# Kernel optimization log

Hardware: AMD Instinct MI355X
Metric: run time of the kernel (lower is better)

Reference implementation:

```python
import jax, jax.numpy as jnp
import numpy as np

D = 64          # lrp_out_dim
L = 16          # lrp_length
LEN_SEQ = 4     # int(sqrt(L))
N = 200000      # nodes
E = 800000      # edges
NPERM = 250000  # permutation patterns
P = NPERM * L   # perm slots (sparse matrix rows)
G = 4096        # graphs (pooling output rows)


def _spmm(row, col, val, m, dense):
    # sparse [m, n] @ dense [n, d] via gather + segment_sum
    return jax.ops.segment_sum(val[:, None] * dense[col], row, num_segments=m)


def setup_inputs() -> dict:
    key = jax.random.key(0)
    ks = jax.random.split(key, 16)
    x = jax.random.normal(ks[0], (N, D), jnp.float32)
    efeat = jax.random.normal(ks[1], (E, D), jnp.float32)
    degs = jax.random.uniform(ks[2], (N,), jnp.float32) * 8.0
    n2p_row = jax.random.randint(ks[3], (P,), 0, P)
    n2p_col = jax.random.randint(ks[4], (P,), 0, N)
    n2p_val = jax.random.uniform(ks[5], (P,), jnp.float32)
    e2p_row = jax.random.randint(ks[6], (P,), 0, P)
    e2p_col = jax.random.randint(ks[7], (P,), 0, E)
    e2p_val = jax.random.uniform(ks[8], (P,), jnp.float32)
    pool_row = jax.random.randint(ks[9], (NPERM,), 0, G)
    pool_col = jax.random.randint(ks[10], (NPERM,), 0, NPERM)
    pool_val = jnp.ones((NPERM,), jnp.float32)
    weights = jax.random.normal(ks[11], (D, D, L), jnp.float32)
    bias = jnp.zeros((1, D), jnp.float32)
    W0 = jax.random.normal(ks[12], (2 * D, LEN_SEQ), jnp.float32) * 0.1
    b0 = jnp.zeros((2 * D,), jnp.float32)
    W1 = jax.random.normal(ks[13], (D, 2 * D), jnp.float32) * 0.1
    b1 = jnp.zeros((D,), jnp.float32)
    Wl = jax.random.normal(ks[14], (D, D), jnp.float32) * 0.1
    bl = jnp.zeros((D,), jnp.float32)
    return dict(x=x, efeat=efeat, degs=degs,
                n2p_row=n2p_row, n2p_col=n2p_col, n2p_val=n2p_val,
                e2p_row=e2p_row, e2p_col=e2p_col, e2p_val=e2p_val,
                pool_row=pool_row, pool_col=pool_col, pool_val=pool_val,
                weights=weights, bias=bias, W0=W0, b0=b0, W1=W1, b1=b1,
                Wl=Wl, bl=bl)


def reference(x, efeat, degs,
              n2p_row, n2p_col, n2p_val,
              e2p_row, e2p_col, e2p_val,
              pool_row, pool_col, pool_val,
              weights, bias, W0, b0, W1, b1, Wl, bl):
    # permutation gather of node and edge features into perm slots: [P, D]
    nfeat = _spmm(n2p_row, n2p_col, n2p_val, P, x) \
          + _spmm(e2p_row, e2p_col, e2p_val, P, efeat)
    deg_perm = _spmm(n2p_row, n2p_col, n2p_val, P, degs[:, None])  # [P, 1]
    # transpose->view->permute in torch is equivalent to a plain reshape here
    nfeat = nfeat.reshape(NPERM, L, D)           # [n_perms, L, D]
    # diagonal-position degree entries: columns 0, 5, 10, 15
    deg_perm = deg_perm.reshape(NPERM, L)[:, jnp.arange(0, L, LEN_SEQ + 1)]  # [n_perms, 4]
    # einsum 'dab,bca->dc' with nfeat [n, a=L, b=D], weights [b=D, c=D, a=L]
    h = jnp.einsum('nlb,bcl->nc', nfeat, weights) + bias
    h = jax.nn.relu(h) @ Wl.T + bl               # self.linear(relu(...))
    dg = jax.nn.relu(deg_perm @ W0.T + b0) @ W1.T + b1  # degree MLP gate
    out = h * dg                                  # [n_perms, D]
    return _spmm(pool_row, pool_col, pool_val, G, out)  # [G, D]
```

## Files before the change

### kernel.cpp

```cpp
#include <hip/hip_runtime.h>

#define NPERM_C 250000
#define P_C     4000000
#define G_C     4096
#define NB1     1954
#define NB2     123

typedef __attribute__((ext_vector_type(8))) short bf16x8;
typedef __attribute__((ext_vector_type(4))) float f32x4;

static __device__ __forceinline__ unsigned short f2bf(float f) {
    unsigned u = __float_as_uint(f);
    unsigned r = (u + 0x7fffu + ((u >> 16) & 1u)) >> 16;
    return (unsigned short)r;
}
static __device__ __forceinline__ float bf2f(unsigned short s) {
    return __uint_as_float(((unsigned)s) << 16);
}

__global__ void repack_bpk(const float* __restrict__ w, unsigned short* __restrict__ bpk) {
    int o = blockIdx.x * 256 + threadIdx.x;
    int j = o & 7, lane = (o >> 3) & 63, h = (o >> 9) & 1;
    int nt = (o >> 10) & 3, ks = (o >> 12) & 1, l = o >> 13;
    int b = ks * 32 + (lane >> 4) * 8 + j;
    int c = nt * 16 + (lane & 15);
    float wv = w[(b * 64 + c) * 16 + l];
    unsigned short hb = f2bf(wv);
    bpk[o] = (h == 0) ? hb : f2bf(wv - bf2f(hb));
}

__global__ void repack_wlpk(const float* __restrict__ wl, unsigned short* __restrict__ wpk) {
    int o = blockIdx.x * 256 + threadIdx.x;
    int j = o & 7, lane = (o >> 3) & 63, h = (o >> 9) & 1;
    int nt = (o >> 10) & 3, ks = o >> 12;
    int k = ks * 32 + (lane >> 4) * 8 + j;
    int c2 = nt * 16 + (lane & 15);
    float wv = wl[c2 * 64 + k];
    unsigned short hb = f2bf(wv);
    wpk[o] = (h == 0) ? hb : f2bf(wv - bf2f(hb));
}

__global__ __launch_bounds__(256) void pool_hist(const int* __restrict__ pcol,
                                                 int* __restrict__ poolCnt) {
    int i = blockIdx.x * 256 + threadIdx.x;
    if (i < NPERM_C) atomicAdd(&poolCnt[pcol[i]], 1);
}

__global__ __launch_bounds__(256) void pool_scan_local(const int* __restrict__ poolCnt,
                                                       int* __restrict__ poolRank,
                                                       int* __restrict__ bsum2) {
    __shared__ int ts[256];
    int b = blockIdx.x, t = threadIdx.x;
    int base = b * 2048 + t * 8;
    int v[8]; int s = 0;
#pragma unroll
    for (int i = 0; i < 8; ++i) {
        int idx = base + i;
        v[i] = (idx < NPERM_C) ? (poolCnt[idx] != 0) : 0;
        s += v[i];
    }
    ts[t] = s;
    __syncthreads();
    for (int ofs = 1; ofs < 256; ofs <<= 1) {
        int xv = (t >= ofs) ? ts[t - ofs] : 0;
        __syncthreads();
        ts[t] += xv;
        __syncthreads();
    }
    int run = ts[t] - s;
    if (t == 255) bsum2[b] = ts[255];
#pragma unroll
    for (int i = 0; i < 8; ++i) {
        int idx = base + i;
        if (idx < NPERM_C) poolRank[idx] = run;
        run += v[i];
    }
}

__global__ void pool_scan_top(int* __restrict__ bsum2) {
    __shared__ int ts[256];
    int t = threadIdx.x;
    int v = (t < NB2) ? bsum2[t] : 0;
    ts[t] = v;
    __syncthreads();
    for (int ofs = 1; ofs < 256; ofs <<= 1) {
        int xv = (t >= ofs) ? ts[t - ofs] : 0;
        __syncthreads();
        ts[t] += xv;
        __syncthreads();
    }
    if (t < NB2) bsum2[t] = ts[t] - v;
}

__global__ __launch_bounds__(256) void pool_scan_add(const int* __restrict__ poolCnt,
                                                     int* __restrict__ poolRank,
                                                     const int* __restrict__ bsum2,
                                                     int* __restrict__ act,
                                                     int* __restrict__ nActB) {
    int b = blockIdx.x, t = threadIdx.x;
    int add = bsum2[b];
    int base = b * 2048 + t * 8;
#pragma unroll
    for (int i = 0; i < 8; ++i) {
        int idx = base + i;
        if (idx < NPERM_C) {
            int flag = poolCnt[idx] != 0;
            int o = poolRank[idx] + add;
            poolRank[idx] = o;
            if (flag) act[o] = idx;
            if (idx == NPERM_C - 1) nActB[0] = o + flag;
        }
    }
}

__global__ __launch_bounds__(256) void hist(const int* __restrict__ r1,
                                            const int* __restrict__ r2,
                                            const int* __restrict__ poolCnt,
                                            int* __restrict__ cnt) {
    int i = blockIdx.x * 256 + threadIdx.x;
    int r;
    if (i < P_C)            r = r1[i];
    else if (i < 2 * P_C)   r = r2[i - P_C];
    else return;
    if (poolCnt[r >> 4] != 0) atomicAdd(&cnt[r], 1);
}

__global__ __launch_bounds__(256) void scan_local(const int* __restrict__ cnt,
                                                  int* __restrict__ off,
                                                  int* __restrict__ bsum) {
    __shared__ int ts[256];
    int b = blockIdx.x, t = threadIdx.x;
    int base = b * 2048 + t * 8;
    int v[8]; int s = 0;
#pragma unroll
    for (int i = 0; i < 8; ++i) {
        int idx = base + i;
        v[i] = (idx < P_C) ? cnt[idx] : 0;
        s += v[i];
    }
    ts[t] = s;
    __syncthreads();
    for (int ofs = 1; ofs < 256; ofs <<= 1) {
        int xv = (t >= ofs) ? ts[t - ofs] : 0;
        __syncthreads();
        ts[t] += xv;
        __syncthreads();
    }
    int run = ts[t] - s;
    if (t == 255) bsum[b] = ts[255];
#pragma unroll
    for (int i = 0; i < 8; ++i) {
        int idx = base + i;
        if (idx < P_C) off[idx] = run;
        run += v[i];
    }
}

__global__ void scan_top(int* __restrict__ bsum) {
    __shared__ int ts[256];
    int t = threadIdx.x;
    int base = t * 8;
    int v[8]; int s = 0;
#pragma unroll
    for (int i = 0; i < 8; ++i) {
        int idx = base + i;
        v[i] = (idx < NB1) ? bsum[idx] : 0;
        s += v[i];
    }
    ts[t] = s;
    __syncthreads();
    for (int ofs = 1; ofs < 256; ofs <<= 1) {
        int xv = (t >= ofs) ? ts[t - ofs] : 0;
        __syncthreads();
        ts[t] += xv;
        __syncthreads();
    }
    int run = ts[t] - s;
#pragma unroll
    for (int i = 0; i < 8; ++i) {
        int idx = base + i;
        if (idx < NB1) bsum[idx] = run;
        run += v[i];
    }
}

__global__ __launch_bounds__(256) void scan_add(int* __restrict__ off,
                                                const int* __restrict__ bsum,
                                                int* __restrict__ cur) {
    int b = blockIdx.x, t = threadIdx.x;
    int add = bsum[b];
    int base = b * 2048 + t * 8;
#pragma unroll
    for (int i = 0; i < 8; ++i) {
        int idx = base + i;
        if (idx < P_C) {
            int o = off[idx] + add;
            if (idx == P_C - 1) off[P_C] = o + cur[idx];
            off[idx] = o;
            cur[idx] = o;
        }
    }
}

__global__ __launch_bounds__(256) void scat(
        const int* __restrict__ r1, const int* __restrict__ c1, const float* __restrict__ v1,
        const int* __restrict__ r2, const int* __restrict__ c2, const float* __restrict__ v2,
        const int* __restrict__ poolCnt,
        int* __restrict__ cur, uint2* __restrict__ suv) {
    int i = blockIdx.x * 256 + threadIdx.x;
    int row; unsigned key; float val;
    if (i < P_C)          { row = r1[i]; key = (unsigned)c1[i]; val = v1[i]; }
    else if (i < 2 * P_C) { int j = i - P_C; row = r2[j]; key = (unsigned)c2[j] | 0x100000u; val = v2[j]; }
    else return;
    if (poolCnt[row >> 4] == 0) return;
    int pos = atomicAdd(&cur[row], 1);
    suv[pos] = make_uint2(key, __float_as_uint(val));
}

__global__ __launch_bounds__(256) void gather_nfeat(
        const uint2* __restrict__ suv, const int* __restrict__ pOff,
        const float* __restrict__ x, const float* __restrict__ efeat,
        const float* __restrict__ degs, const int* __restrict__ act,
        const int* __restrict__ nActB,
        unsigned short* __restrict__ nfH, unsigned short* __restrict__ nfL,
        float* __restrict__ degD, int row0, int rows) {
    int nAct = nActB[0];
    int t = threadIdx.x;
    int w = t >> 6, lane = t & 63;
    int g = lane >> 4, t16 = lane & 15;
    int cr = row0 + blockIdx.x * 2 + (w >> 1);
    int rend = row0 + rows; if (rend > nAct) rend = nAct;
    if (cr >= rend) return;
    int arow = act[cr];
    int posA = (w & 1) * 8 + g * 2;
    int posB = posA + 1;
    int sA = arow * 16 + posA;
    int iA = pOff[sA];
    int eA = pOff[sA + 1];
    int iB = eA;
    int eB = pOff[sA + 2];
    bool needA = (posA == 0) || (posA == 10);
    bool needB = (posB == 5) || (posB == 15);
    float4 aA = {0.f, 0.f, 0.f, 0.f}, aB = {0.f, 0.f, 0.f, 0.f};
    float dA = 0.f, dB = 0.f;
    while ((iA < eA) || (iB < eB)) {
        bool hA = iA < eA, hB = iB < eB;
        uint2 kvA, kvB;
        if (hA) kvA = suv[iA];
        if (hB) kvB = suv[iB];
        if (hA) {
            unsigned k = kvA.x; float v = __uint_as_float(kvA.y);
            const float* f = (k & 0x100000u) ? efeat : x;
            float4 fv = *reinterpret_cast<const float4*>(
                f + (size_t)(k & 0xFFFFFu) * 64 + t16 * 4);
            aA.x = fmaf(v, fv.x, aA.x); aA.y = fmaf(v, fv.y, aA.y);
            aA.z = fmaf(v, fv.z, aA.z); aA.w = fmaf(v, fv.w, aA.w);
            if (needA && !(k & 0x100000u)) dA = fmaf(v, degs[k & 0xFFFFFu], dA);
            ++iA;
        }
        if (hB) {
            unsigned k = kvB.x; float v = __uint_as_float(kvB.y);
            const float* f = (k & 0x100000u) ? efeat : x;
            float4 fv = *reinterpret_cast<const float4*>(
                f + (size_t)(k & 0xFFFFFu) * 64 + t16 * 4);
            aB.x = fmaf(v, fv.x, aB.x); aB.y = fmaf(v, fv.y, aB.y);
            aB.z = fmaf(v, fv.z, aB.z); aB.w = fmaf(v, fv.w, aB.w);
            if (needB && !(k & 0x100000u)) dB = fmaf(v, degs[k & 0xFFFFFu], dB);
            ++iB;
        }
    }
    size_t o = ((size_t)(cr - row0) * 16 + posA) * 64 + t16 * 4;
    ushort4 h4, l4;
    h4.x = f2bf(aA.x); l4.x = f2bf(aA.x - bf2f(h4.x));
    h4.y = f2bf(aA.y); l4.y = f2bf(aA.y - bf2f(h4.y));
    h4.z = f2bf(aA.z); l4.z = f2bf(aA.z - bf2f(h4.z));
    h4.w = f2bf(aA.w); l4.w = f2bf(aA.w - bf2f(h4.w));
    *reinterpret_cast<ushort4*>(nfH + o) = h4;
    *reinterpret_cast<ushort4*>(nfL + o) = l4;
    h4.x = f2bf(aB.x); l4.x = f2bf(aB.x - bf2f(h4.x));
    h4.y = f2bf(aB.y); l4.y = f2bf(aB.y - bf2f(h4.y));
    h4.z = f2bf(aB.z); l4.z = f2bf(aB.z - bf2f(h4.z));
    h4.w = f2bf(aB.w); l4.w = f2bf(aB.w - bf2f(h4.w));
    *reinterpret_cast<ushort4*>(nfH + o + 64) = h4;
    *reinterpret_cast<ushort4*>(nfL + o + 64) = l4;
    if (t16 == 0) {
        if (needA) degD[(size_t)cr * 4 + posA / 5] = dA;
        if (needB) degD[(size_t)cr * 4 + posB / 5] = dB;
    }
}

__global__ __launch_bounds__(256) void dg_gemm(
        const float* __restrict__ degD,
        const float* __restrict__ W0, const float* __restrict__ b0,
        const float* __restrict__ W1, const float* __restrict__ b1,
        const int* __restrict__ nActB,
        float* __restrict__ dgb, int r0, int rows) {
    __shared__ float hidT[128][68];
    __shared__ float w1T[128][68];
    __shared__ float dloc[64][4];
    __shared__ float w0s[128][5];
    int nAct = nActB[0];
    int rend = r0 + rows; if (rend > nAct) rend = nAct;
    int t = threadIdx.x;
    int m0 = r0 + blockIdx.x * 64;
    if (m0 >= rend) return;

    {
        int r = t >> 2, j = t & 3;
        int gr = m0 + r; if (gr >= rend) gr = rend - 1;
        dloc[r][j] = degD[(size_t)gr * 4 + j];
    }
    if (t < 128) {
        w0s[t][0] = W0[t * 4 + 0]; w0s[t][1] = W0[t * 4 + 1];
        w0s[t][2] = W0[t * 4 + 2]; w0s[t][3] = W0[t * 4 + 3];
        w0s[t][4] = b0[t];
    }
    for (int s = 0; s < 32; ++s) {
        int idx = t + s * 256;
        w1T[idx & 127][idx >> 7] = W1[idx];
    }
    __syncthreads();
    for (int s = 0; s < 32; ++s) {
        int idx = t + s * 256;
        int h = idx & 127, r = idx >> 7;
        float v = w0s[h][4] + dloc[r][0] * w0s[h][0] + dloc[r][1] * w0s[h][1]
                            + dloc[r][2] * w0s[h][2] + dloc[r][3] * w0s[h][3];
        hidT[h][r] = fmaxf(v, 0.f);
    }
    __syncthreads();

    int tm = t >> 4, tn = t & 15;
    float acc[4][4] = {};
#pragma unroll 8
    for (int k = 0; k < 128; ++k) {
        float4 a = *reinterpret_cast<const float4*>(&hidT[k][tm * 4]);
        float4 b = *reinterpret_cast<const float4*>(&w1T[k][tn * 4]);
        acc[0][0] = fmaf(a.x, b.x, acc[0][0]); acc[0][1] = fmaf(a.x, b.y, acc[0][1]);
        acc[0][2] = fmaf(a.x, b.z, acc[0][2]); acc[0][3] = fmaf(a.x, b.w, acc[0][3]);
        acc[1][0] = fmaf(a.y, b.x, acc[1][0]); acc[1][1] = fmaf(a.y, b.y, acc[1][1]);
        acc[1][2] = fmaf(a.y, b.z, acc[1][2]); acc[1][3] = fmaf(a.y, b.w, acc[1][3]);
        acc[2][0] = fmaf(a.z, b.x, acc[2][0]); acc[2][1] = fmaf(a.z, b.y, acc[2][1]);
        acc[2][2] = fmaf(a.z, b.z, acc[2][2]); acc[2][3] = fmaf(a.z, b.w, acc[2][3]);
        acc[3][0] = fmaf(a.w, b.x, acc[3][0]); acc[3][1] = fmaf(a.w, b.y, acc[3][1]);
        acc[3][2] = fmaf(a.w, b.z, acc[3][2]); acc[3][3] = fmaf(a.w, b.w, acc[3][3]);
    }
    float bb[4] = {b1[tn * 4 + 0], b1[tn * 4 + 1], b1[tn * 4 + 2], b1[tn * 4 + 3]};
#pragma unroll
    for (int i = 0; i < 4; ++i) {
        int grow = m0 + tm * 4 + i;
        if (grow < rend) {
            float4 o = {acc[i][0] + bb[0], acc[i][1] + bb[1],
                        acc[i][2] + bb[2], acc[i][3] + bb[3]};
            *reinterpret_cast<float4*>(&dgb[(size_t)grow * 64 + tn * 4]) = o;
        }
    }
}

__global__ __launch_bounds__(256) void gemm_mfma(
        const unsigned short* __restrict__ nfH, const unsigned short* __restrict__ nfL,
        const unsigned short* __restrict__ Bpk, const unsigned short* __restrict__ Wlpk,
        const float* __restrict__ bias, const float* __restrict__ bl,
        const float* __restrict__ dgb, const int* __restrict__ nActB,
        float* __restrict__ outb, int r0, int rows) {
    __shared__ unsigned short Hh[128][72];
    __shared__ unsigned short Hl[128][72];
    int nAct = nActB[0];
    int rowsEff = rows; if (r0 + rowsEff > nAct) rowsEff = nAct - r0;
    int t = threadIdx.x, lane = t & 63, w = t >> 6;
    int m0 = blockIdx.x * 128;
    if (m0 >= rowsEff) return;
    int r16 = lane & 15, kg = lane >> 4;

    f32x4 acc[2][4];
#pragma unroll
    for (int i = 0; i < 2; ++i)
#pragma unroll
        for (int j = 0; j < 4; ++j) acc[i][j] = (f32x4){0.f, 0.f, 0.f, 0.f};

    for (int l = 0; l < 16; ++l) {
#pragma unroll
        for (int ks = 0; ks < 2; ++ks) {
            bf16x8 ah[2], al[2];
#pragma unroll
            for (int mt = 0; mt < 2; ++mt) {
                int lr = m0 + w * 32 + mt * 16 + r16;
                if (lr >= rowsEff) lr = rowsEff - 1;
                size_t off = ((size_t)lr * 16 + l) * 64 + ks * 32 + kg * 8;
                ah[mt] = *reinterpret_cast<const bf16x8*>(nfH + off);
                al[mt] = *reinterpret_cast<const bf16x8*>(nfL + off);
            }
#pragma unroll
            for (int nt = 0; nt < 4; ++nt) {
                const unsigned short* bb =
                    Bpk + (size_t)(((l * 2 + ks) * 4 + nt) * 2) * 512 + lane * 8;
                bf16x8 bh = *reinterpret_cast<const bf16x8*>(bb);
                bf16x8 blo = *reinterpret_cast<const bf16x8*>(bb + 512);
#pragma unroll
                for (int mt = 0; mt < 2; ++mt) {
                    acc[mt][nt] = __builtin_amdgcn_mfma_f32_16x16x32_bf16(ah[mt], bh,  acc[mt][nt], 0, 0, 0);
                    acc[mt][nt] = __builtin_amdgcn_mfma_f32_16x16x32_bf16(ah[mt], blo, acc[mt][nt], 0, 0, 0);
                    acc[mt][nt] = __builtin_amdgcn_mfma_f32_16x16x32_bf16(al[mt], bh,  acc[mt][nt], 0, 0, 0);
                }
            }
        }
    }

#pragma unroll
    for (int mt = 0; mt < 2; ++mt)
#pragma unroll
        for (int nt = 0; nt < 4; ++nt) {
            int col = nt * 16 + r16;
            float bv = bias[col];
#pragma unroll
            for (int reg = 0; reg < 4; ++reg) {
                int rl = w * 32 + mt * 16 + kg * 4 + reg;
                float h = fmaxf(acc[mt][nt][reg] + bv, 0.f);
                unsigned short hb = f2bf(h);
                Hh[rl][col] = hb;
                Hl[rl][col] = f2bf(h - bf2f(hb));
            }
        }
    __syncthreads();

    f32x4 acc2[2][4];
#pragma unroll
    for (int i = 0; i < 2; ++i)
#pragma unroll
        for (int j = 0; j < 4; ++j) acc2[i][j] = (f32x4){0.f, 0.f, 0.f, 0.f};

#pragma unroll
    for (int ks = 0; ks < 2; ++ks) {
        bf16x8 ah[2], al[2];
#pragma unroll
        for (int mt = 0; mt < 2; ++mt) {
            int rl = w * 32 + mt * 16 + r16;
            ah[mt] = *reinterpret_cast<const bf16x8*>(&Hh[rl][ks * 32 + kg * 8]);
            al[mt] = *reinterpret_cast<const bf16x8*>(&Hl[rl][ks * 32 + kg * 8]);
        }
#pragma unroll
        for (int nt = 0; nt < 4; ++nt) {
            const unsigned short* wb =
                Wlpk + (size_t)(((ks * 4 + nt) * 2)) * 512 + lane * 8;
            bf16x8 bh = *reinterpret_cast<const bf16x8*>(wb);
            bf16x8 blo = *reinterpret_cast<const bf16x8*>(wb + 512);
#pragma unroll
            for (int mt = 0; mt < 2; ++mt) {
                acc2[mt][nt] = __builtin_amdgcn_mfma_f32_16x16x32_bf16(ah[mt], bh,  acc2[mt][nt], 0, 0, 0);
                acc2[mt][nt] = __builtin_amdgcn_mfma_f32_16x16x32_bf16(ah[mt], blo, acc2[mt][nt], 0, 0, 0);
                acc2[mt][nt] = __builtin_amdgcn_mfma_f32_16x16x32_bf16(al[mt], bh,  acc2[mt][nt], 0, 0, 0);
            }
        }
    }

#pragma unroll
    for (int mt = 0; mt < 2; ++mt)
#pragma unroll
        for (int nt = 0; nt < 4; ++nt) {
            int col = nt * 16 + r16;
            float bv = bl[col];
#pragma unroll
            for (int reg = 0; reg < 4; ++reg) {
                int rl = w * 32 + mt * 16 + kg * 4 + reg;
                if (m0 + rl < rowsEff) {
                    size_t idx = (size_t)(r0 + m0 + rl) * 64 + col;
                    outb[idx] = (acc2[mt][nt][reg] + bv) * dgb[idx];
                }
            }
        }
}

__global__ __launch_bounds__(256) void pool_scatter(
        const int* __restrict__ prow, const int* __restrict__ pcol,
        const float* __restrict__ pval, const int* __restrict__ poolRank,
        const float* __restrict__ outb, float* __restrict__ out) {
    int t = blockIdx.x * 256 + threadIdx.x;
    int i = t >> 6, d = t & 63;
    if (i >= NPERM_C) return;
    int r = prow[i], c = pcol[i];
    float v = pval[i];
    int cr = poolRank[c];
    atomicAdd(&out[(size_t)r * 64 + d], v * outb[(size_t)cr * 64 + d]);
}

extern "C" void kernel_launch(void* const* d_in, const int* in_sizes, int n_in,
                              void* d_out, int out_size, void* d_ws, size_t ws_size,
                              hipStream_t stream) {
    const float* x       = (const float*)d_in[0];
    const float* efeat   = (const float*)d_in[1];
    const float* degs    = (const float*)d_in[2];
    const int*   n2p_row = (const int*)d_in[3];
    const int*   n2p_col = (const int*)d_in[4];
    const float* n2p_val = (const float*)d_in[5];
    const int*   e2p_row = (const int*)d_in[6];
    const int*   e2p_col = (const int*)d_in[7];
    const float* e2p_val = (const float*)d_in[8];
    const int*   pool_row = (const int*)d_in[9];
    const int*   pool_col = (const int*)d_in[10];
    const float* pool_val = (const float*)d_in[11];
    const float* weights = (const float*)d_in[12];
    const float* bias    = (const float*)d_in[13];
    const float* W0      = (const float*)d_in[14];
    const float* b0      = (const float*)d_in[15];
    const float* W1      = (const float*)d_in[16];
    const float* b1      = (const float*)d_in[17];
    const float* Wl      = (const float*)d_in[18];
    const float* bl      = (const float*)d_in[19];
    float* out = (float*)d_out;

    uint2* suv      = (uint2*)d_ws;
    int*   pOff     = (int*)(suv + 8000000);
    int*   pCur     = pOff + 4000064;
    int*   bsum     = pCur + 4000000;
    int*   poolCnt  = bsum + 2048;
    int*   poolRank = poolCnt + 250000;
    int*   act      = poolRank + 250000;
    int*   bsum2    = act + 250000;
    int*   nActB    = bsum2 + 256;
    unsigned short* Bpk  = (unsigned short*)(nActB + 16);
    unsigned short* Wlpk = Bpk + 131072;
    float* degD = (float*)(Wlpk + 8192);
    float* dgb  = degD + 1000000;
    float* outb = dgb;
    unsigned short* nfH = (unsigned short*)(dgb + 16000000);

    const long long base_elems = 16000000LL + 4000064 + 4000000 + 2048 +
                                 250000 * 3 + 256 + 16 + 65536 + 4096 +
                                 1000000 + 16000000;
    long long availf = (long long)(ws_size / 4) - base_elems;
    long long chl = availf / 1024;
    if (chl > NPERM_C) chl = NPERM_C;
    int CH = (int)(chl & ~127LL);
    if (CH < 128) {
        hipMemsetAsync(d_out, 0, (size_t)out_size * 4, stream);
        return;
    }
    unsigned short* nfL = nfH + (size_t)CH * 1024;

    hipMemsetAsync(pCur, 0, (size_t)P_C * 4, stream);
    hipMemsetAsync(poolCnt, 0, (size_t)NPERM_C * 4, stream);
    hipMemsetAsync(out, 0, (size_t)G_C * 64 * 4, stream);

    repack_bpk<<<512, 256, 0, stream>>>(weights, Bpk);
    repack_wlpk<<<32, 256, 0, stream>>>(Wl, Wlpk);

    pool_hist<<<(NPERM_C + 255) / 256, 256, 0, stream>>>(pool_col, poolCnt);
    pool_scan_local<<<NB2, 256, 0, stream>>>(poolCnt, poolRank, bsum2);
    pool_scan_top<<<1, 256, 0, stream>>>(bsum2);
    pool_scan_add<<<NB2, 256, 0, stream>>>(poolCnt, poolRank, bsum2, act, nActB);

    hist<<<31250, 256, 0, stream>>>(n2p_row, e2p_row, poolCnt, pCur);
    scan_local<<<NB1, 256, 0, stream>>>(pCur, pOff, bsum);
    scan_top<<<1, 256, 0, stream>>>(bsum);
    scan_add<<<NB1, 256, 0, stream>>>(pOff, bsum, pCur);
    scat<<<31250, 256, 0, stream>>>(n2p_row, n2p_col, n2p_val,
                                    e2p_row, e2p_col, e2p_val,
                                    poolCnt, pCur, suv);

    for (int c0 = 0; c0 < NPERM_C; c0 += CH) {
        int rows = NPERM_C - c0; if (rows > CH) rows = CH;
        gather_nfeat<<<(rows + 1) / 2, 256, 0, stream>>>(
            suv, pOff, x, efeat, degs, act, nActB, nfH, nfL, degD, c0, rows);
        dg_gemm<<<(rows + 63) / 64, 256, 0, stream>>>(
            degD, W0, b0, W1, b1, nActB, dgb, c0, rows);
        gemm_mfma<<<(rows + 127) / 128, 256, 0, stream>>>(
            nfH, nfL, Bpk, Wlpk, bias, bl, dgb, nActB, outb, c0, rows);
    }

    pool_scatter<<<62500, 256, 0, stream>>>(pool_row, pool_col, pool_val,
                                            poolRank, outb, out);
}
```

Measured before the change: 1.494 ms.

## Balance gather_nfeat work per perm row using shared-memory atomic accumulation

gather_nfeat now processes 8 perm rows per block. Each row's full nonzero range is split across two 16-lane groups, which accumulate into a 32KB shared-memory tile with LDS float atomics instead of per-slot register accumulators. The goal is to remove the load imbalance of the old one-group-per-two-slots loop, where lanes idled while the longest slot finished. The cost is shared atomics, a linear scan to find each entry's slot, more LDS per block (so lower occupancy), and extra block-wide syncs.

```diff
diff --git a/kernel.cpp b/kernel.cpp
--- a/kernel.cpp
+++ b/kernel.cpp
@@ -224,68 +224,75 @@
         const int* __restrict__ nActB,
         unsigned short* __restrict__ nfH, unsigned short* __restrict__ nfL,
         float* __restrict__ degD, int row0, int rows) {
+    __shared__ float accS[8192];
+    __shared__ int   offS[8][17];
+    __shared__ int   arowS[8];
+    __shared__ float degS[8][4];
     int nAct = nActB[0];
     int t = threadIdx.x;
-    int w = t >> 6, lane = t & 63;
-    int g = lane >> 4, t16 = lane & 15;
-    int cr = row0 + blockIdx.x * 2 + (w >> 1);
+    int cr0 = row0 + blockIdx.x * 8;
     int rend = row0 + rows; if (rend > nAct) rend = nAct;
-    if (cr >= rend) return;
-    int arow = act[cr];
-    int posA = (w & 1) * 8 + g * 2;
-    int posB = posA + 1;
-    int sA = arow * 16 + posA;
-    int iA = pOff[sA];
-    int eA = pOff[sA + 1];
-    int iB = eA;
-    int eB = pOff[sA + 2];
-    bool needA = (posA == 0) || (posA == 10);
-    bool needB = (posB == 5) || (posB == 15);
-    float4 aA = {0.f, 0.f, 0.f, 0.f}, aB = {0.f, 0.f, 0.f, 0.f};
-    float dA = 0.f, dB = 0.f;
-    while ((iA < eA) || (iB < eB)) {
-        bool hA = iA < eA, hB = iB < eB;
-        uint2 kvA, kvB;
-        if (hA) kvA = suv[iA];
-        if (hB) kvB = suv[iB];
-        if (hA) {
-            unsigned k = kvA.x; float v = __uint_as_float(kvA.y);
+    if (cr0 >= rend) return;
+
+    if (t < 8) arowS[t] = (cr0 + t < rend) ? act[cr0 + t] : -1;
+    __syncthreads();
+    if (t < 136) {
+        int r = t / 17, j = t - r * 17;
+        int ar = arowS[r];
+        offS[r][j] = (ar >= 0) ? pOff[ar * 16 + j] : 0;
+    }
+#pragma unroll
+    for (int i = 0; i < 32; ++i) accS[t + i * 256] = 0.f;
+    if (t < 32) degS[t >> 2][t & 3] = 0.f;
+    __syncthreads();
+
+    {
+        int w = t >> 6;
+        int g = (t >> 4) & 3;
+        int t16 = t & 15;
+        int r = w * 2 + (g >> 1);
+        int par = g & 1;
+        int e0 = offS[r][0], e1 = offS[r][16];
+        int s = 0;
+        for (int e = e0 + par; e < e1; e += 2) {
+            while (s < 15 && e >= offS[r][s + 1]) ++s;
+            uint2 kv = suv[e];
+            unsigned k = kv.x;
+            float v = __uint_as_float(kv.y);
             const float* f = (k & 0x100000u) ? efeat : x;
             float4 fv = *reinterpret_cast<const float4*>(
                 f + (size_t)(k & 0xFFFFFu) * 64 + t16 * 4);
-            aA.x = fmaf(v, fv.x, aA.x); aA.y = fmaf(v, fv.y, aA.y);
-            aA.z = fmaf(v, fv.z, aA.z); aA.w = fmaf(v, fv.w, aA.w);
-            if (needA && !(k & 0x100000u)) dA = fmaf(v, degs[k & 0xFFFFFu], dA);
-            ++iA;
-        }
-        if (hB) {
-            unsigned k = kvB.x; float v = __uint_as_float(kvB.y);
-            const float* f = (k & 0x100000u) ? efeat : x;
-            float4 fv = *reinterpret_cast<const float4*>(
-                f + (size_t)(k & 0xFFFFFu) * 64 + t16 * 4);
-            aB.x = fmaf(v, fv.x, aB.x); aB.y = fmaf(v, fv.y, aB.y);
-            aB.z = fmaf(v, fv.z, aB.z); aB.w = fmaf(v, fv.w, aB.w);
-            if (needB && !(k & 0x100000u)) dB = fmaf(v, degs[k & 0xFFFFFu], dB);
-            ++iB;
-        }
-    }
-    size_t o = ((size_t)(cr - row0) * 16 + posA) * 64 + t16 * 4;
-    ushort4 h4, l4;
-    h4.x = f2bf(aA.x); l4.x = f2bf(aA.x - bf2f(h4.x));
-    h4.y = f2bf(aA.y); l4.y = f2bf(aA.y - bf2f(h4.y));
-    h4.z = f2bf(aA.z); l4.z = f2bf(aA.z - bf2f(h4.z));
-    h4.w = f2bf(aA.w); l4.w = f2bf(aA.w - bf2f(h4.w));
-    *reinterpret_cast<ushort4*>(nfH + o) = h4;
-    *reinterpret_cast<ushort4*>(nfL + o) = l4;
-    h4.x = f2bf(aB.x); l4.x = f2bf(aB.x - bf2f(h4.x));
-    h4.y = f2bf(aB.y); l4.y = f2bf(aB.y - bf2f(h4.y));
-    h4.z = f2bf(aB.z); l4.z = f2bf(aB.z - bf2f(h4.z));
-    h4.w = f2bf(aB.w); l4.w = f2bf(aB.w - bf2f(h4.w));
-    *reinterpret_cast<ushort4*>(nfH + o + 64) = h4;
-    *reinterpret_cast<ushort4*>(nfL + o + 64) = l4;
-    if (t16 == 0) {
-        if (needA) degD[(size_t)cr * 4 + posA / 5] = dA;
-        if (needB) degD[(size_t)cr * 4 + posB / 5] = dB;
+            float* dst = &accS[(r * 16 + s) * 64 + t16 * 4];
+            atomicAdd(dst + 0, v * fv.x);
+            atomicAdd(dst + 1, v * fv.y);
+            atomicAdd(dst + 2, v * fv.z);
+            atomicAdd(dst + 3, v * fv.w);
+            if (t16 == 0 && !(k & 0x100000u)) {
+                if (s == 0 || s == 5 || s == 10 || s == 15)
+                    atomicAdd(&degS[r][s / 5], v * degs[k & 0xFFFFFu]);
+            }
+        }
+    }
+    __syncthreads();
+
+    size_t nfbase = (size_t)(cr0 - row0) * 1024;
+#pragma unroll
+    for (int it = 0; it < 8; ++it) {
+        if (cr0 + it >= rend) break;
+        int flat = it * 1024 + t * 4;
+        float4 a = *reinterpret_cast<const float4*>(&accS[flat]);
+        ushort4 h4, l4;
+        h4.x = f2bf(a.x); l4.x = f2bf(a.x - bf2f(h4.x));
+        h4.y = f2bf(a.y); l4.y = f2bf(a.y - bf2f(h4.y));
+        h4.z = f2bf(a.z); l4.z = f2bf(a.z - bf2f(h4.z));
+        h4.w = f2bf(a.w); l4.w = f2bf(a.w - bf2f(h4.w));
+        *reinterpret_cast<ushort4*>(nfH + nfbase + flat) = h4;
+        *reinterpret_cast<ushort4*>(nfL + nfbase + flat) = l4;
+    }
+    if (t < 32) {
+        int r2 = t >> 2;
+        if (cr0 + r2 < rend)
+            degD[(size_t)(cr0 + r2) * 4 + (t & 3)] = degS[r2][t & 3];
     }
 }
 
@@ -558,7 +565,7 @@
 
     for (int c0 = 0; c0 < NPERM_C; c0 += CH) {
         int rows = NPERM_C - c0; if (rows > CH) rows = CH;
-        gather_nfeat<<<(rows + 1) / 2, 256, 0, stream>>>(
+        gather_nfeat<<<(rows + 7) / 8, 256, 0, stream>>>(
             suv, pOff, x, efeat, degs, act, nActB, nfH, nfL, degD, c0, rows);
         dg_gemm<<<(rows + 63) / 64, 256, 0, stream>>>(
             degD, W0, b0, W1, b1, nActB, dgb, c0, rows);
```

Result: slower. 2.656 ms (+77.7%).

## Compact CSR rows to active permutation order and cap chunk size

Applied to the files above, without the earlier changes.

Encodes the active flag and compacted rank in one poolRk word, so hist and scat index the CSR counters by compacted row instead of the original perm row. gather_nfeat then reads pOff contiguously by compacted row, and the act indirection array is removed. It also caps the chunk size at 32768 permutations so the per-chunk intermediates stay smaller and more cache-resident. The trade-off is extra kernel launches from the cap, plus a small decode cost on every lookup.

```diff
diff --git a/kernel.cpp b/kernel.cpp
--- a/kernel.cpp
+++ b/kernel.cpp
@@ -47,7 +47,7 @@
 }
 
 __global__ __launch_bounds__(256) void pool_scan_local(const int* __restrict__ poolCnt,
-                                                       int* __restrict__ poolRank,
+                                                       int* __restrict__ poolRk,
                                                        int* __restrict__ bsum2) {
     __shared__ int ts[256];
     int b = blockIdx.x, t = threadIdx.x;
@@ -72,7 +72,7 @@
 #pragma unroll
     for (int i = 0; i < 8; ++i) {
         int idx = base + i;
-        if (idx < NPERM_C) poolRank[idx] = run;
+        if (idx < NPERM_C) poolRk[idx] = run;
         run += v[i];
     }
 }
@@ -93,9 +93,8 @@
 }
 
 __global__ __launch_bounds__(256) void pool_scan_add(const int* __restrict__ poolCnt,
-                                                     int* __restrict__ poolRank,
+                                                     int* __restrict__ poolRk,
                                                      const int* __restrict__ bsum2,
-                                                     int* __restrict__ act,
                                                      int* __restrict__ nActB) {
     int b = blockIdx.x, t = threadIdx.x;
     int add = bsum2[b];
@@ -105,9 +104,8 @@
         int idx = base + i;
         if (idx < NPERM_C) {
             int flag = poolCnt[idx] != 0;
-            int o = poolRank[idx] + add;
-            poolRank[idx] = o;
-            if (flag) act[o] = idx;
+            int o = poolRk[idx] + add;
+            poolRk[idx] = (o << 1) | flag;
             if (idx == NPERM_C - 1) nActB[0] = o + flag;
         }
     }
@@ -115,14 +113,15 @@
 
 __global__ __launch_bounds__(256) void hist(const int* __restrict__ r1,
                                             const int* __restrict__ r2,
-                                            const int* __restrict__ poolCnt,
+                                            const int* __restrict__ poolRk,
                                             int* __restrict__ cnt) {
     int i = blockIdx.x * 256 + threadIdx.x;
     int r;
     if (i < P_C)            r = r1[i];
     else if (i < 2 * P_C)   r = r2[i - P_C];
     else return;
-    if (poolCnt[r >> 4] != 0) atomicAdd(&cnt[r], 1);
+    int info = poolRk[r >> 4];
+    if (info & 1) atomicAdd(&cnt[(info >> 1) * 16 + (r & 15)], 1);
 }
 
 __global__ __launch_bounds__(256) void scan_local(const int* __restrict__ cnt,
@@ -205,23 +204,23 @@
 __global__ __launch_bounds__(256) void scat(
         const int* __restrict__ r1, const int* __restrict__ c1, const float* __restrict__ v1,
         const int* __restrict__ r2, const int* __restrict__ c2, const float* __restrict__ v2,
-        const int* __restrict__ poolCnt,
+        const int* __restrict__ poolRk,
         int* __restrict__ cur, uint2* __restrict__ suv) {
     int i = blockIdx.x * 256 + threadIdx.x;
     int row; unsigned key; float val;
     if (i < P_C)          { row = r1[i]; key = (unsigned)c1[i]; val = v1[i]; }
     else if (i < 2 * P_C) { int j = i - P_C; row = r2[j]; key = (unsigned)c2[j] | 0x100000u; val = v2[j]; }
     else return;
-    if (poolCnt[row >> 4] == 0) return;
-    int pos = atomicAdd(&cur[row], 1);
+    int info = poolRk[row >> 4];
+    if (!(info & 1)) return;
+    int pos = atomicAdd(&cur[(info >> 1) * 16 + (row & 15)], 1);
     suv[pos] = make_uint2(key, __float_as_uint(val));
 }
 
 __global__ __launch_bounds__(256) void gather_nfeat(
         const uint2* __restrict__ suv, const int* __restrict__ pOff,
         const float* __restrict__ x, const float* __restrict__ efeat,
-        const float* __restrict__ degs, const int* __restrict__ act,
-        const int* __restrict__ nActB,
+        const float* __restrict__ degs, const int* __restrict__ nActB,
         unsigned short* __restrict__ nfH, unsigned short* __restrict__ nfL,
         float* __restrict__ degD, int row0, int rows) {
     int nAct = nActB[0];
@@ -231,10 +230,9 @@
     int cr = row0 + blockIdx.x * 2 + (w >> 1);
     int rend = row0 + rows; if (rend > nAct) rend = nAct;
     if (cr >= rend) return;
-    int arow = act[cr];
     int posA = (w & 1) * 8 + g * 2;
     int posB = posA + 1;
-    int sA = arow * 16 + posA;
+    int sA = cr * 16 + posA;
     int iA = pOff[sA];
     int eA = pOff[sA + 1];
     int iB = eA;
@@ -471,14 +469,14 @@
 
 __global__ __launch_bounds__(256) void pool_scatter(
         const int* __restrict__ prow, const int* __restrict__ pcol,
-        const float* __restrict__ pval, const int* __restrict__ poolRank,
+        const float* __restrict__ pval, const int* __restrict__ poolRk,
         const float* __restrict__ outb, float* __restrict__ out) {
     int t = blockIdx.x * 256 + threadIdx.x;
     int i = t >> 6, d = t & 63;
     if (i >= NPERM_C) return;
     int r = prow[i], c = pcol[i];
     float v = pval[i];
-    int cr = poolRank[c];
+    int cr = poolRk[c] >> 1;
     atomicAdd(&out[(size_t)r * 64 + d], v * outb[(size_t)cr * 64 + d]);
 }
 
@@ -512,9 +510,8 @@
     int*   pCur     = pOff + 4000064;
     int*   bsum     = pCur + 4000000;
     int*   poolCnt  = bsum + 2048;
-    int*   poolRank = poolCnt + 250000;
-    int*   act      = poolRank + 250000;
-    int*   bsum2    = act + 250000;
+    int*   poolRk   = poolCnt + 250000;
+    int*   bsum2    = poolRk + 250000;
     int*   nActB    = bsum2 + 256;
     unsigned short* Bpk  = (unsigned short*)(nActB + 16);
     unsigned short* Wlpk = Bpk + 131072;
@@ -524,12 +521,13 @@
     unsigned short* nfH = (unsigned short*)(dgb + 16000000);
 
     const long long base_elems = 16000000LL + 4000064 + 4000000 + 2048 +
-                                 250000 * 3 + 256 + 16 + 65536 + 4096 +
+                                 250000 * 2 + 256 + 16 + 65536 + 4096 +
                                  1000000 + 16000000;
     long long availf = (long long)(ws_size / 4) - base_elems;
     long long chl = availf / 1024;
     if (chl > NPERM_C) chl = NPERM_C;
     int CH = (int)(chl & ~127LL);
+    if (CH > 32768) CH = 32768;
     if (CH < 128) {
         hipMemsetAsync(d_out, 0, (size_t)out_size * 4, stream);
         return;
@@ -544,22 +542,22 @@
     repack_wlpk<<<32, 256, 0, stream>>>(Wl, Wlpk);
 
     pool_hist<<<(NPERM_C + 255) / 256, 256, 0, stream>>>(pool_col, poolCnt);
-    pool_scan_local<<<NB2, 256, 0, stream>>>(poolCnt, poolRank, bsum2);
+    pool_scan_local<<<NB2, 256, 0, stream>>>(poolCnt, poolRk, bsum2);
     pool_scan_top<<<1, 256, 0, stream>>>(bsum2);
-    pool_scan_add<<<NB2, 256, 0, stream>>>(poolCnt, poolRank, bsum2, act, nActB);
-
-    hist<<<31250, 256, 0, stream>>>(n2p_row, e2p_row, poolCnt, pCur);
+    pool_scan_add<<<NB2, 256, 0, stream>>>(poolCnt, poolRk, bsum2, nActB);
+
+    hist<<<31250, 256, 0, stream>>>(n2p_row, e2p_row, poolRk, pCur);
     scan_local<<<NB1, 256, 0, stream>>>(pCur, pOff, bsum);
     scan_top<<<1, 256, 0, stream>>>(bsum);
     scan_add<<<NB1, 256, 0, stream>>>(pOff, bsum, pCur);
     scat<<<31250, 256, 0, stream>>>(n2p_row, n2p_col, n2p_val,
                                     e2p_row, e2p_col, e2p_val,
-                                    poolCnt, pCur, suv);
+                                    poolRk, pCur, suv);
 
     for (int c0 = 0; c0 < NPERM_C; c0 += CH) {
         int rows = NPERM_C - c0; if (rows > CH) rows = CH;
         gather_nfeat<<<(rows + 1) / 2, 256, 0, stream>>>(
-            suv, pOff, x, efeat, degs, act, nActB, nfH, nfL, degD, c0, rows);
+            suv, pOff, x, efeat, degs, nActB, nfH, nfL, degD, c0, rows);
         dg_gemm<<<(rows + 63) / 64, 256, 0, stream>>>(
             degD, W0, b0, W1, b1, nActB, dgb, c0, rows);
         gemm_mfma<<<(rows + 127) / 128, 256, 0, stream>>>(
@@ -567,5 +565,5 @@
     }
 
     pool_scatter<<<62500, 256, 0, stream>>>(pool_row, pool_col, pool_val,
-                                            poolRank, outb, out);
-}
+                                            poolRk, outb, out);
+}
```

Result: slower. 1.659 ms (+11.0%).
